# Kernel tuning notes

Measured on AMD Instinct MI355X. Metric: run time of the kernel, lower is better.

## Reference

```python
import jax, jax.numpy as jnp
import numpy as np

EMBED_DIM = 1024
NUM_HEADS = 16
NUM_GROUPS = 4
HEAD_DIM = EMBED_DIM // NUM_HEADS          # 64
KV_REPEAT = NUM_HEADS // NUM_GROUPS        # 4
KV_DIM = HEAD_DIM * NUM_GROUPS             # 256


def setup_inputs() -> dict:
    key = jax.random.key(0)
    ks = jax.random.split(key, 9)
    s = 0.02
    x = jax.random.normal(ks[0], (4, 2048, EMBED_DIM), dtype=jnp.float32)
    Wq = jax.random.normal(ks[1], (EMBED_DIM, EMBED_DIM), dtype=jnp.float32) * s
    bq = jnp.zeros((EMBED_DIM,), dtype=jnp.float32)
    Wk = jax.random.normal(ks[2], (EMBED_DIM, KV_DIM), dtype=jnp.float32) * s
    bk = jnp.zeros((KV_DIM,), dtype=jnp.float32)
    Wv = jax.random.normal(ks[3], (EMBED_DIM, KV_DIM), dtype=jnp.float32) * s
    bv = jnp.zeros((KV_DIM,), dtype=jnp.float32)
    Wo = jax.random.normal(ks[4], (EMBED_DIM, EMBED_DIM), dtype=jnp.float32) * s
    bo = jnp.zeros((EMBED_DIM,), dtype=jnp.float32)
    return {"x": x, "Wq": Wq, "bq": bq, "Wk": Wk, "bk": bk,
            "Wv": Wv, "bv": bv, "Wo": Wo, "bo": bo}


def reference(x, Wq, bq, Wk, bk, Wv, bv, Wo, bo):
    B, S, E = x.shape
    G, R, D = NUM_GROUPS, KV_REPEAT, HEAD_DIM
    scale = 1.0 / jnp.sqrt(jnp.float32(D))
    # projections
    q = (x @ Wq + bq).reshape(B, S, G, R, D)   # query head h = g*R + r, matching
    k = (x @ Wk + bk).reshape(B, S, G, D)      # torch repeat_interleave grouping
    v = (x @ Wv + bv).reshape(B, S, G, D)
    # scaled scores: [B, G, R, Sq, Sk] -- same O(n^2) math, no KV duplication
    scores = jnp.einsum('bqgrd,bkgd->bgrqk', q * scale, k)
    attn = jax.nn.softmax(scores, axis=-1)
    out = jnp.einsum('bgrqk,bkgd->bqgrd', attn, v).reshape(B, S, E)
    return out @ Wo + bo
```

## Files before the change

### kernel.cpp

```cpp
#include <hip/hip_runtime.h>
#include <hip/hip_bf16.h>
#include <cstdint>


#define B_  4
#define S_  2048
#define E_  1024
#define H_  16
#define G_  4
#define R_  4
#define D_  64
#define KV_ 256

typedef unsigned short u16;
typedef unsigned int u32;
typedef __attribute__((ext_vector_type(8))) __bf16 bf16x8;
typedef __attribute__((ext_vector_type(4))) float f32x4;

#if __has_builtin(__builtin_amdgcn_exp2f)
#define EXP2(x) __builtin_amdgcn_exp2f(x)
#else
#define EXP2(x) exp2f(x)
#endif

__device__ __forceinline__ float b2f(u16 v) {
    unsigned u = ((unsigned)v) << 16;
    return __builtin_bit_cast(float, u);
}
__device__ __forceinline__ u16 f2b(float f) {
    unsigned u = __builtin_bit_cast(unsigned, f);
    u += 0x7fffu + ((u >> 16) & 1u);
    return (u16)(u >> 16);
}
__device__ __forceinline__ u16 f2b_rtz(float f) {
    return (u16)(__builtin_bit_cast(unsigned, f) >> 16);
}

__device__ __forceinline__ int sniff_f32(const u16* w, int t) {
    bool hit = (w[t & 63] & 0x4000) != 0;
    return (__popcll(__ballot(hit)) > 4) ? 1 : 0;
}

__device__ __forceinline__ void gl_lds16(const u16* g, u16* l) {
    __builtin_amdgcn_global_load_lds(
        (const __attribute__((address_space(1))) u32*)(const void*)g,
        (__attribute__((address_space(3))) u32*)(void*)l, 16, 0, 0);
}

__global__ __launch_bounds__(256) void prep_all(
    const void* __restrict__ x,
    const void* __restrict__ Wq, const void* __restrict__ Wk,
    const void* __restrict__ Wv, const void* __restrict__ Wo,
    u16* __restrict__ xc, u16* __restrict__ WqT, u16* __restrict__ WkT,
    u16* __restrict__ WvT, u16* __restrict__ WoT)
{
    __shared__ u16 tile[64][65];
    const int f = sniff_f32((const u16*)Wq, threadIdx.x);
    int b = blockIdx.x;
    if (b < 4096) {
        int i0 = (b * 256 + threadIdx.x) * 8;
        if (f) {
            const float4* s = (const float4*)x;
            float4 a = s[i0 / 4], c = s[i0 / 4 + 1];
            uint4 o;
            o.x = (u32)f2b(a.x) | ((u32)f2b(a.y) << 16);
            o.y = (u32)f2b(a.z) | ((u32)f2b(a.w) << 16);
            o.z = (u32)f2b(c.x) | ((u32)f2b(c.y) << 16);
            o.w = (u32)f2b(c.z) | ((u32)f2b(c.w) << 16);
            *(uint4*)(xc + i0) = o;
        } else {
            *(uint4*)(xc + i0) = ((const uint4*)x)[i0 / 8];
        }
        return;
    }
    int j = b - 4096;
    const void* src; u16* dst; int N, nt, kt;
    if (j < 256)      {           src = Wq; dst = WqT; N = 1024; nt = j & 15; kt = j >> 4; }
    else if (j < 320) { j -= 256; src = Wk; dst = WkT; N = 256;  nt = j & 3;  kt = j >> 2; }
    else if (j < 384) { j -= 320; src = Wv; dst = WvT; N = 256;  nt = j & 3;  kt = j >> 2; }
    else              { j -= 384; src = Wo; dst = WoT; N = 1024; nt = j & 15; kt = j >> 4; }
    const int K = 1024;
    const int n0 = nt * 64, k0 = kt * 64;
    const int tr = threadIdx.x >> 6, tc = threadIdx.x & 63;
#pragma unroll
    for (int i = 0; i < 16; i++) {
        int k = k0 + i * 4 + tr;
        size_t idx = (size_t)k * N + n0 + tc;
        float v = f ? ((const float*)src)[idx] : b2f(((const u16*)src)[idx]);
        tile[i * 4 + tr][tc] = f2b(v);
    }
    __syncthreads();
#pragma unroll
    for (int i = 0; i < 16; i++) {
        int n = n0 + i * 4 + tr;
        dst[(size_t)n * K + k0 + tc] = tile[tc][i * 4 + tr];
    }
}

__device__ __forceinline__ float load_bias(const void* b, int i, int f) {
    return f ? ((const float*)b)[i] : b2f(((const u16*)b)[i]);
}

__global__ __launch_bounds__(512, 4) void gemm_bt(
    const u16* __restrict__ A, const u16* __restrict__ Bt,
    const void* __restrict__ bA, const void* __restrict__ bB,
    const void* __restrict__ bC,
    void* __restrict__ Cv, void* __restrict__ Cv2, void* __restrict__ Cv3,
    int M, int N, int K, int mode, const u16* __restrict__ sniffw)
{
    __shared__ __align__(16) u16 As[128][64];
    __shared__ __align__(16) u16 Bs[128][64];

    const int t    = threadIdx.x;
    const int wave = t >> 6, lane = t & 63;
    const int lr   = lane & 15, quad = lane >> 4;
    const int kgrp = quad * 8;
    const int m0 = blockIdx.y * 128, n0 = blockIdx.x * 128;
    const int wm = (wave >> 1) * 32, wn = (wave & 1) * 64;
    const int f = sniff_f32(sniffw, t);

    f32x4 acc[2][4];
#pragma unroll
    for (int i = 0; i < 2; i++)
#pragma unroll
        for (int j = 0; j < 4; j++) acc[i][j] = (f32x4){0.f, 0.f, 0.f, 0.f};

    for (int k0 = 0; k0 < K; k0 += 64) {
#pragma unroll
        for (int i = 0; i < 2; i++) {
            int c = t + i * 512;
            int row = c >> 3, cc = (c & 7) * 8;
            int lbase = (i * 512 + wave * 64) * 8;
            gl_lds16(A  + (size_t)(m0 + row) * K + k0 + cc, &As[0][0] + lbase);
            gl_lds16(Bt + (size_t)(n0 + row) * K + k0 + cc, &Bs[0][0] + lbase);
        }
        __syncthreads();
#pragma unroll
        for (int s2 = 0; s2 < 2; ++s2) {
            bf16x8 af[2], bfr[4];
#pragma unroll
            for (int tm = 0; tm < 2; tm++)
                af[tm] = *(const bf16x8*)&As[wm + tm * 16 + lr][s2 * 32 + kgrp];
#pragma unroll
            for (int tn = 0; tn < 4; tn++)
                bfr[tn] = *(const bf16x8*)&Bs[wn + tn * 16 + lr][s2 * 32 + kgrp];
#pragma unroll
            for (int tm = 0; tm < 2; tm++)
#pragma unroll
                for (int tn = 0; tn < 4; tn++)
                    acc[tm][tn] = __builtin_amdgcn_mfma_f32_16x16x32_bf16(
                        af[tm], bfr[tn], acc[tm][tn], 0, 0, 0);
        }
        __syncthreads();
    }

#pragma unroll
    for (int tm = 0; tm < 2; tm++) {
        int rowb = m0 + wm + tm * 16 + quad * 4;
#pragma unroll
        for (int tn = 0; tn < 4; tn++) {
            int col = n0 + wn + tn * 16 + lr;
            float bv;
            if (mode == 2)           bv = load_bias(bA, col, f);
            else if (col < 1024)     bv = load_bias(bA, col, f);
            else if (col < 1280)     bv = load_bias(bB, col - 1024, f);
            else                     bv = load_bias(bC, col - 1280, f);
            if (mode == 4 && col >= 1280) {
                int c2 = col - 1280, g = c2 >> 6, d = c2 & 63;
                int bi = rowb >> 11, s = rowb & 2047;
                u16 h[4];
#pragma unroll
                for (int r = 0; r < 4; r++) h[r] = f2b(acc[tm][tn][r] + bv);
                uint2 pk;
                pk.x = (u32)h[0] | ((u32)h[1] << 16);
                pk.y = (u32)h[2] | ((u32)h[3] << 16);
                *(uint2*)&((u16*)Cv3)[((size_t)(bi * G_ + g) * D_ + d) * S_ + s] = pk;
                continue;
            }
#pragma unroll
            for (int r = 0; r < 4; r++) {
                int row = rowb + r;
                float val = acc[tm][tn][r] + bv;
                if (mode == 2) {
                    if (f) ((float*)Cv)[(size_t)row * N + col] = val;
                    else   ((u16*)Cv)[(size_t)row * N + col] = f2b(val);
                } else if (col < 1024) {
                    ((u16*)Cv)[(size_t)row * 1024 + col] = f2b(val * 0.18033688f);
                } else {
                    ((u16*)Cv2)[(size_t)row * 256 + (col - 1024)] = f2b(val);
                }
            }
        }
    }
}

__global__ __launch_bounds__(512, 4) void flash_gqa(
    const u16* __restrict__ Q, const u16* __restrict__ Kb,
    const u16* __restrict__ Vt, u16* __restrict__ AO)
{
    __shared__ __align__(16) u16 Ks[64][72];
    __shared__ __align__(16) u16 Vs[64][72];
    __shared__ __align__(16) u16 Ps[8][32][40];

    const int t    = threadIdx.x;
    const int wave = t >> 6, lane = t & 63;
    const int lr   = lane & 15, quad = lane >> 4, kgrp = quad * 8;

    const int bg = blockIdx.x;
    const int bi = bg / G_, g = bg % G_;
    const int h  = g * R_ + (wave & 3);
    const int sq0 = blockIdx.y * 64 + (wave >> 2) * 32;

    const u16* qp   = Q  + ((size_t)bi * S_ + sq0) * E_ + h * D_;
    const u16* kptr = Kb + (size_t)bi * S_ * KV_ + g * D_;
    const u16* vptr = Vt + (size_t)(bi * G_ + g) * D_ * S_;
    u16 (*Pw)[40] = Ps[wave];

    bf16x8 aq[2][2];
#pragma unroll
    for (int tm = 0; tm < 2; tm++)
#pragma unroll
        for (int s2 = 0; s2 < 2; s2++)
            aq[tm][s2] = *(const bf16x8*)(qp + (size_t)(tm * 16 + lr) * E_ + s2 * 32 + kgrp);

    float rs[8];
    f32x4 o[2][4];
#pragma unroll
    for (int i = 0; i < 8; i++) rs[i] = 0.f;
#pragma unroll
    for (int i = 0; i < 2; i++)
#pragma unroll
        for (int j = 0; j < 4; j++) o[i][j] = (f32x4){0.f, 0.f, 0.f, 0.f};

    const int srow = t >> 3, scol = (t & 7) * 8;
    const u16* kg = kptr + (size_t)srow * KV_ + scol;
    const u16* vg = vptr + (size_t)srow * S_ + scol;

    for (int j = 0; j < S_ / 64; j++) {
        __syncthreads();
        int kb = j * 64;
        *(uint4*)&Ks[srow][scol] = *(const uint4*)(kg + (size_t)kb * KV_);
        *(uint4*)&Vs[srow][scol] = *(const uint4*)(vg + kb);
        __syncthreads();

#pragma unroll
        for (int h2 = 0; h2 < 2; h2++) {
#pragma unroll
            for (int tn2 = 0; tn2 < 2; tn2++) {
                int tn = h2 * 2 + tn2;
                f32x4 sc[2];
#pragma unroll
                for (int a = 0; a < 2; a++) sc[a] = (f32x4){0.f, 0.f, 0.f, 0.f};
                __builtin_amdgcn_s_setprio(1);
#pragma unroll
                for (int s2 = 0; s2 < 2; ++s2) {
                    bf16x8 bk = *(const bf16x8*)&Ks[tn * 16 + lr][s2 * 32 + kgrp];
#pragma unroll
                    for (int tm = 0; tm < 2; tm++)
                        sc[tm] = __builtin_amdgcn_mfma_f32_16x16x32_bf16(
                            aq[tm][s2], bk, sc[tm], 0, 0, 0);
                }
                __builtin_amdgcn_s_setprio(0);
#pragma unroll
                for (int tm = 0; tm < 2; tm++)
#pragma unroll
                    for (int r = 0; r < 4; r++) {
                        float p = EXP2(sc[tm][r]);
                        Pw[tm * 16 + quad * 4 + r][tn2 * 16 + lr] = f2b_rtz(p);
                        rs[tm * 4 + r] += p;
                    }
            }
            bf16x8 ap[2], bv[4];
#pragma unroll
            for (int tm = 0; tm < 2; tm++)
                ap[tm] = *(const bf16x8*)&Pw[tm * 16 + lr][kgrp];
#pragma unroll
            for (int td = 0; td < 4; td++)
                bv[td] = *(const bf16x8*)&Vs[td * 16 + lr][h2 * 32 + kgrp];
            __builtin_amdgcn_s_setprio(1);
#pragma unroll
            for (int tm = 0; tm < 2; tm++)
#pragma unroll
                for (int td = 0; td < 4; td++)
                    o[tm][td] = __builtin_amdgcn_mfma_f32_16x16x32_bf16(
                        ap[tm], bv[td], o[tm][td], 0, 0, 0);
            __builtin_amdgcn_s_setprio(0);
        }
    }

#pragma unroll
    for (int msk = 1; msk < 16; msk <<= 1)
#pragma unroll
        for (int i = 0; i < 8; i++) rs[i] += __shfl_xor(rs[i], msk);

#pragma unroll
    for (int tm = 0; tm < 2; tm++)
#pragma unroll
        for (int r = 0; r < 4; r++) {
            int s = sq0 + tm * 16 + quad * 4 + r;
            float inv = 1.0f / fmaxf(rs[tm * 4 + r], 1e-30f);
#pragma unroll
            for (int td = 0; td < 4; td++) {
                int d = td * 16 + lr;
                AO[(((size_t)bi * S_ + s) * H_ + h) * D_ + d] = f2b(o[tm][td][r] * inv);
            }
        }
}

extern "C" void kernel_launch(void* const* d_in, const int* in_sizes, int n_in,
                              void* d_out, int out_size, void* d_ws, size_t ws_size,
                              hipStream_t stream) {
    const void* x  = d_in[0];
    const void* Wq = d_in[1];
    const void* bq = d_in[2];
    const void* Wk = d_in[3];
    const void* bk = d_in[4];
    const void* Wv = d_in[5];
    const void* bv = d_in[6];
    const void* Wo = d_in[7];
    const void* bo = d_in[8];

    u16* ws  = (u16*)d_ws;
    u16* xc  = ws;
    u16* WqT = xc  + (size_t)8388608;
    u16* WkT = WqT + 1048576;
    u16* WvT = WkT + 262144;
    u16* WoT = WvT + 262144;
    u16* Qb  = WoT + 1048576;
    u16* Kb  = Qb  + (size_t)8388608;
    u16* Vtb = Kb  + (size_t)2097152;
    u16* AO  = Vtb + (size_t)2097152;

    size_t need = 2ull * ((size_t)(AO - ws) + 8388608ull);
    if (ws_size < need) return;

    prep_all<<<4736, 256, 0, stream>>>(x, Wq, Wk, Wv, Wo,
                                       xc, WqT, WkT, WvT, WoT);

    dim3 blk(512);
    gemm_bt<<<dim3(1536 / 128, 8192 / 128), blk, 0, stream>>>(
        xc, WqT, bq, bk, bv, Qb, Kb, Vtb, 8192, 1536, 1024, 4, (const u16*)Wq);
    flash_gqa<<<dim3(B_ * G_, S_ / 64), blk, 0, stream>>>(Qb, Kb, Vtb, AO);
    gemm_bt<<<dim3(1024 / 128, 8192 / 128), blk, 0, stream>>>(
        AO, WoT, bo, nullptr, nullptr, d_out, nullptr, nullptr,
        8192, 1024, 1024, 2, (const u16*)Wq);
}
```

Measured before the change: 267.4 us.

## Double-buffer LDS tiles in GEMM to overlap global loads with MFMA

Splits the shared-memory A/B tiles into two buffers and prefetches the tile two steps ahead with direct global-to-LDS loads, using a partial vmcnt wait plus raw s_barrier instead of __syncthreads. This is meant to hide global memory latency behind the MFMA work. In exchange, LDS use per block doubles to 64KB, which may cut occupancy below the declared 4 blocks per CU, and the hand-counted vmcnt(4) depends on how many loads each stage issues.

```diff
diff --git a/kernel.cpp b/kernel.cpp
--- a/kernel.cpp
+++ b/kernel.cpp
@@ -108,8 +108,8 @@
     void* __restrict__ Cv, void* __restrict__ Cv2, void* __restrict__ Cv3,
     int M, int N, int K, int mode, const u16* __restrict__ sniffw)
 {
-    __shared__ __align__(16) u16 As[128][64];
-    __shared__ __align__(16) u16 Bs[128][64];
+    __shared__ __align__(16) u16 As[2][128][64];
+    __shared__ __align__(16) u16 Bs[2][128][64];
 
     const int t    = threadIdx.x;
     const int wave = t >> 6, lane = t & 63;
@@ -125,25 +125,26 @@
 #pragma unroll
         for (int j = 0; j < 4; j++) acc[i][j] = (f32x4){0.f, 0.f, 0.f, 0.f};
 
-    for (int k0 = 0; k0 < K; k0 += 64) {
+    auto stage = [&](int buf, int k0) {
 #pragma unroll
         for (int i = 0; i < 2; i++) {
             int c = t + i * 512;
             int row = c >> 3, cc = (c & 7) * 8;
             int lbase = (i * 512 + wave * 64) * 8;
-            gl_lds16(A  + (size_t)(m0 + row) * K + k0 + cc, &As[0][0] + lbase);
-            gl_lds16(Bt + (size_t)(n0 + row) * K + k0 + cc, &Bs[0][0] + lbase);
-        }
-        __syncthreads();
+            gl_lds16(A  + (size_t)(m0 + row) * K + k0 + cc, &As[buf][0][0] + lbase);
+            gl_lds16(Bt + (size_t)(n0 + row) * K + k0 + cc, &Bs[buf][0][0] + lbase);
+        }
+    };
+    auto compute = [&](const u16 (*Asb)[64], const u16 (*Bsb)[64]) {
 #pragma unroll
         for (int s2 = 0; s2 < 2; ++s2) {
             bf16x8 af[2], bfr[4];
 #pragma unroll
             for (int tm = 0; tm < 2; tm++)
-                af[tm] = *(const bf16x8*)&As[wm + tm * 16 + lr][s2 * 32 + kgrp];
+                af[tm] = *(const bf16x8*)&Asb[wm + tm * 16 + lr][s2 * 32 + kgrp];
 #pragma unroll
             for (int tn = 0; tn < 4; tn++)
-                bfr[tn] = *(const bf16x8*)&Bs[wn + tn * 16 + lr][s2 * 32 + kgrp];
+                bfr[tn] = *(const bf16x8*)&Bsb[wn + tn * 16 + lr][s2 * 32 + kgrp];
 #pragma unroll
             for (int tm = 0; tm < 2; tm++)
 #pragma unroll
@@ -151,8 +152,29 @@
                     acc[tm][tn] = __builtin_amdgcn_mfma_f32_16x16x32_bf16(
                         af[tm], bfr[tn], acc[tm][tn], 0, 0, 0);
         }
-        __syncthreads();
-    }
+    };
+
+    const int NT = K >> 6;
+    stage(0, 0);
+    if (NT > 1) stage(1, 64);
+    int cur = 0;
+    for (int kt = 0; kt < NT - 1; kt++) {
+        asm volatile("s_waitcnt vmcnt(4)" ::: "memory");
+        __builtin_amdgcn_sched_barrier(0);
+        __builtin_amdgcn_s_barrier();
+        __builtin_amdgcn_sched_barrier(0);
+        compute(As[cur], Bs[cur]);
+        __builtin_amdgcn_sched_barrier(0);
+        __builtin_amdgcn_s_barrier();
+        __builtin_amdgcn_sched_barrier(0);
+        if (kt + 2 < NT) stage(cur, (kt + 2) * 64);
+        cur ^= 1;
+    }
+    asm volatile("s_waitcnt vmcnt(0)" ::: "memory");
+    __builtin_amdgcn_sched_barrier(0);
+    __builtin_amdgcn_s_barrier();
+    __builtin_amdgcn_sched_barrier(0);
+    compute(As[cur], Bs[cur]);
 
 #pragma unroll
     for (int tm = 0; tm < 2; tm++) {
```

Result: slower. 284.0 us (+6.2%).
